# Optimization experiments

Measured on AMD Instinct MI355X. Metric: run time of the kernel, lower is better.

The kernel has to match this reference:

```python
import math
import jax, jax.numpy as jnp
import numpy as np

B, H, W, C = 2, 32, 32, 64
K = 15
G = 4
GC = C // G
K2 = K * K
RED = C // 4
MAX_SIGMA = 0.5


def setup_inputs() -> dict:
    key = jax.random.key(0)
    ks = jax.random.split(key, 32)
    f32 = jnp.float32

    def rn(k, shape, std):
        return (jax.random.normal(k, shape) * std).astype(f32)

    lin = 1.0 / math.sqrt(C)
    inp = {
        'x': jax.random.normal(ks[0], (B, H, W, C), f32),
        'raw_sigma': jnp.asarray(math.log(math.exp(0.3) - 1.0), f32),
        'base_offset_scale': jnp.asarray(0.1, f32),
        # input/output projections (stored [in,out])
        'w_ip': rn(ks[1], (C, C), lin), 'b_ip': jnp.zeros((C,), f32),
        'w_op': rn(ks[2], (C, C), lin), 'b_op': jnp.zeros((C,), f32),
        # dw_conv: depthwise 3x3 (HWIO, I=1) then pointwise 1x1 ([in,out])
        'w_dw': rn(ks[3], (3, 3, 1, C), 1.0 / 3.0), 'b_dw': jnp.zeros((C,), f32),
        'w_pw': rn(ks[4], (C, C), lin), 'b_pw': jnp.zeros((C,), f32),
        # offset / mask heads (original zero-inits; small random to exercise path)
        'w_off': rn(ks[5], (C, G * K2 * 2), 0.01), 'b_off': rn(ks[6], (G * K2 * 2,), 0.01),
        'w_msk': rn(ks[7], (C, G * K2), 0.01), 'b_msk': rn(ks[8], (G * K2,), 0.01),
        # kernel MLP: 2 -> 32 -> 32 -> G*GC
        'w_k1': rn(ks[9], (2, 32), 0.5), 'b_k1': jnp.zeros((32,), f32),
        'w_k2': rn(ks[10], (32, 32), 1.0 / math.sqrt(32)), 'b_k2': jnp.zeros((32,), f32),
        'w_k3': rn(ks[11], (32, G * GC), 1.0 / math.sqrt(32)), 'b_k3': jnp.zeros((G * GC,), f32),
        # SE block
        'w_fc1': rn(ks[12], (C, RED), lin), 'b_fc1': jnp.zeros((RED,), f32),
        'w_fc2': rn(ks[13], (RED, C), 1.0 / math.sqrt(RED)), 'b_fc2': jnp.zeros((C,), f32),
    }
    return inp


def _forward(x, raw_sigma, base_offset_scale, w_ip, b_ip, w_op, b_op, w_dw, b_dw,
             w_pw, b_pw, w_off, b_off, w_msk, b_msk, w_k1, b_k1, w_k2, b_k2,
             w_k3, b_k3, w_fc1, b_fc1, w_fc2, b_fc2):
    Bx, Hx, Wx, Cx = x.shape
    sigma = jnp.clip(jax.nn.softplus(raw_sigma), 1e-3, MAX_SIGMA)
    grid = jnp.linspace(-0.5, 0.5, K)  # [K]

    x_proj = x @ w_ip + b_ip  # [B,H,W,C]

    # depthwise 3x3 (SAME) + SiLU + pointwise 1x1
    y = jax.lax.conv_general_dilated(
        x, w_dw, (1, 1), 'SAME',
        dimension_numbers=('NHWC', 'HWIO', 'NHWC'), feature_group_count=Cx) + b_dw
    x_dw = jax.nn.silu(y) @ w_pw + b_pw  # [B,H,W,C]

    # Gaussian envelope over kernel grid, normalized
    env = jnp.exp(-(grid[:, None] ** 2 + grid[None, :] ** 2) / (2.0 * sigma ** 2))
    env = env / jnp.maximum(env.sum(), 1e-8)
    env_flat = env.reshape(1, 1, 1, 1, K2)

    gh, gw = jnp.meshgrid(grid, grid, indexing='ij')
    pos = jnp.stack([gh.ravel(), gw.ravel()], axis=-1) * 2.0  # [K2,2]
    hkw = jax.nn.silu(pos @ w_k1 + b_k1)
    hkw = jax.nn.silu(hkw @ w_k2 + b_k2)
    kw_raw = hkw @ w_k3 + b_k3  # [K2, G*GC]
    # faithful to torch view quirk: (K,K,G,gc) memory reinterpreted as (G,K2,gc)
    kw = kw_raw.reshape(G, K2, GC).reshape(1, 1, 1, G, K2, GC)

    offsets = (x_dw @ w_off + b_off).reshape(Bx, Hx, Wx, G, K2, 2) * base_offset_scale
    raw_mask = (x_dw @ w_msk + b_msk).reshape(Bx, Hx, Wx, G, K2) * env_flat
    attn = jnp.nan_to_num(jax.nn.softmax(raw_mask, axis=-1))

    # absolute sampling locations
    ref = jnp.linspace(-(K // 2), K // 2, K)
    rh, rw = jnp.meshgrid(ref, ref, indexing='ij')  # [K,K]
    pos_h = jnp.arange(Hx, dtype=x.dtype).reshape(1, Hx, 1, 1, 1)
    pos_w = jnp.arange(Wx, dtype=x.dtype).reshape(1, 1, Wx, 1, 1)
    abs_h = pos_h + rh.ravel().reshape(1, 1, 1, 1, K2) + offsets[..., 0]
    abs_w = pos_w + rw.ravel().reshape(1, 1, 1, 1, K2) + offsets[..., 1]
    ah = jnp.clip(abs_h, 0.0, Hx - 1)
    aw = jnp.clip(abs_w, 0.0, Wx - 1)
    h_f = jnp.clip(jnp.floor(ah).astype(jnp.int32), 0, Hx - 1)
    w_f = jnp.clip(jnp.floor(aw).astype(jnp.int32), 0, Wx - 1)
    h_c = jnp.minimum(h_f + 1, Hx - 1)
    w_c = jnp.minimum(w_f + 1, Wx - 1)
    hw = ah - h_f.astype(x.dtype)
    ww = aw - w_f.astype(x.dtype)
    valid = (~((abs_h < 0) | (abs_h > Hx - 1) | (abs_w < 0) | (abs_w > Wx - 1))).astype(x.dtype)

    xg = x_proj.reshape(Bx, Hx, Wx, G, GC)
    b_idx = jnp.arange(Bx).reshape(Bx, 1, 1, 1, 1)
    g_idx = jnp.arange(G).reshape(1, 1, 1, G, 1)
    v_ff = xg[b_idx, h_f, w_f, g_idx]  # [B,H,W,G,K2,GC]
    v_fc = xg[b_idx, h_f, w_c, g_idx]
    v_cf = xg[b_idx, h_c, w_f, g_idx]
    v_cc = xg[b_idx, h_c, w_c, g_idx]
    sampled = (v_ff * ((1 - hw) * (1 - ww) * valid)[..., None]
               + v_fc * ((1 - hw) * ww * valid)[..., None]
               + v_cf * (hw * (1 - ww) * valid)[..., None]
               + v_cc * (hw * ww * valid)[..., None])
    sampled = sampled * kw
    output = (sampled * attn[..., None]).sum(axis=4).reshape(Bx, Hx, Wx, Cx)

    # SE block (no mask, no bias)
    pooled = output.mean(axis=(1, 2), keepdims=True)
    se = jax.nn.silu(pooled @ w_fc1 + b_fc1) @ w_fc2 + b_fc2
    output = output * jax.nn.sigmoid(se)

    out = output @ w_op + b_op
    offset_reg = (offsets ** 2).mean()
    entropy = -(attn * jnp.log(attn + 1e-8)).sum(axis=-1).mean()
    return out, offset_reg, -entropy


def reference(x, raw_sigma, base_offset_scale, w_ip, b_ip, w_op, b_op, w_dw, b_dw,
              w_pw, b_pw, w_off, b_off, w_msk, b_msk, w_k1, b_k1, w_k2, b_k2,
              w_k3, b_k3, w_fc1, b_fc1, w_fc2, b_fc2):
    return _forward(x, raw_sigma, base_offset_scale, w_ip, b_ip, w_op, b_op,
                    w_dw, b_dw, w_pw, b_pw, w_off, b_off, w_msk, b_msk,
                    w_k1, b_k1, w_k2, b_k2, w_k3, b_k3, w_fc1, b_fc1, w_fc2, b_fc2)
```

## Files before the change

kernel.cpp:

```cpp
#include <hip/hip_runtime.h>
#include <math.h>

#define KK2 225
#define NPIX 2048
#define OFFC 1800
#define MSKC 900
#define NCOL 2700
#define NCOLP 2704
#define HSTR 2704

#define WROW 17
#define WCOL 20
#define WPOS (WROW*WCOL)
#define WSTR 68

#define WS_KW    0
#define WS_XPROJ 16384
#define WS_XB    (16384+131072)
#define WS_OUT   (16384+2*131072)
#define WS_POOL  (16384+3*131072)
#define WS_GATE  (WS_POOL+128)
#define WS_ENTP  (WS_GATE+128)
#define WS_OFFP  (WS_ENTP+2048)
#define WS_PART2 (WS_OFFP+512)
#define WS_WB    (WS_PART2+4096)
#define WS_HD    (WS_WB+86528)

typedef __attribute__((ext_vector_type(8))) short short8;
typedef __attribute__((ext_vector_type(4))) float f32x4;

__device__ __forceinline__ float silu(float a) { return a / (1.f + __expf(-a)); }
__device__ __forceinline__ unsigned short f2bf(float f) {
  unsigned u = __float_as_uint(f);
  u += 0x7FFFu + ((u >> 16) & 1u);
  return (unsigned short)(u >> 16);
}
__device__ __forceinline__ float bf2f(unsigned short h) {
  return __uint_as_float(((unsigned)h) << 16);
}

__global__ __launch_bounds__(256) void k_pre(
    const float* __restrict__ x,
    const float* __restrict__ w_ip, const float* __restrict__ b_ip,
    const float* __restrict__ w_dw, const float* __restrict__ b_dw,
    const float* __restrict__ w_pw, const float* __restrict__ b_pw,
    const float* __restrict__ w_k1, const float* __restrict__ b_k1,
    const float* __restrict__ w_k2, const float* __restrict__ b_k2,
    const float* __restrict__ w_k3, const float* __restrict__ b_k3,
    const float* __restrict__ w_off, const float* __restrict__ w_msk,
    float* __restrict__ ws)
{
  int t = threadIdx.x;
  if (blockIdx.x < 512) {
    int px = t >> 6, c = t & 63;
    int pix = blockIdx.x * 4 + px;
    int b = pix >> 10, h = (pix >> 5) & 31, w = pix & 31;
    __shared__ float xs[4][64], ys[4][64];
    xs[px][c] = x[pix*64 + c];
    float acc = b_dw[c];
    #pragma unroll
    for (int dh = -1; dh <= 1; dh++) {
      int hh = h + dh;
      if (hh < 0 || hh > 31) continue;
      #pragma unroll
      for (int dw2 = -1; dw2 <= 1; dw2++) {
        int wp = w + dw2;
        if (wp < 0 || wp > 31) continue;
        acc += x[(((b*32 + hh)*32 + wp) << 6) + c] * w_dw[((dh+1)*3 + (dw2+1))*64 + c];
      }
    }
    ys[px][c] = silu(acc);
    __syncthreads();
    float p1 = b_ip[c], p2 = b_pw[c];
    #pragma unroll 8
    for (int k = 0; k < 64; k++) {
      p1 += xs[px][k] * w_ip[k*64 + c];
      p2 += ys[px][k] * w_pw[k*64 + c];
    }
    ((unsigned short*)(ws + WS_XPROJ))[pix*64 + c] = f2bf(p1);
    ((unsigned short*)(ws + WS_XB))[pix*64 + c]    = f2bf(p2);
  } else if (blockIdx.x < 569) {
    __shared__ float h1s[4][32], h2s[4][32];
    int tl = t >> 6, lane = t & 63;
    int tap = (blockIdx.x - 512) * 4 + tl;
    int tapc = min(tap, KK2 - 1);
    int i = tapc / 15, j = tapc % 15;
    float gi = -0.5f + (float)i * (1.0f/14.0f);
    float gj = -0.5f + (float)j * (1.0f/14.0f);
    float p0 = gi * 2.f, p1 = gj * 2.f;
    if (lane < 32) {
      float a = p0 * w_k1[lane] + p1 * w_k1[32 + lane] + b_k1[lane];
      h1s[tl][lane] = silu(a);
    }
    __syncthreads();
    if (lane < 32) {
      float a = b_k2[lane];
      #pragma unroll
      for (int q = 0; q < 32; q++) a += h1s[tl][q] * w_k2[q*32 + lane];
      h2s[tl][lane] = silu(a);
    }
    __syncthreads();
    float a = b_k3[lane];
    #pragma unroll
    for (int q = 0; q < 32; q++) a += h2s[tl][q] * w_k3[q*64 + lane];
    if (tap < KK2) ws[WS_KW + tap*64 + lane] = a;
  } else {
    unsigned short* wb = (unsigned short*)(ws + WS_WB);
    int cb = blockIdx.x - 569;
    int col = cb*16 + (t & 15);
    int kk = (t >> 4) * 4;
    unsigned short v4[4];
    #pragma unroll
    for (int j = 0; j < 4; j++) {
      int k = kk + j;
      float v = 0.f;
      if (col < OFFC)      v = w_off[k*OFFC + col];
      else if (col < NCOL) v = w_msk[k*MSKC + col - OFFC];
      v4[j] = f2bf(v);
    }
    *(uint2*)&wb[(size_t)col*64 + kk] = *(uint2*)v4;
  }
}

__global__ __launch_bounds__(256) void k_gemm(
    const float* __restrict__ base_scale,
    const float* __restrict__ b_off, const float* __restrict__ b_msk,
    float* __restrict__ ws)
{
  int t = threadIdx.x;
  int wv = t >> 6, lane = t & 63;
  int row = lane & 15, rg = lane >> 4;
  int k0 = rg * 8;
  int colb = blockIdx.x * 64;
  int pxb  = blockIdx.y * 64 + wv * 16;
  const unsigned short* xb = (const unsigned short*)(ws + WS_XB);
  const unsigned short* wb = (const unsigned short*)(ws + WS_WB);
  unsigned short* hd = (unsigned short*)(ws + WS_HD);
  float scale = base_scale[0];

  short8 a_lo = *(const short8*)&xb[(size_t)(pxb + row)*64 + k0];
  short8 a_hi = *(const short8*)&xb[(size_t)(pxb + row)*64 + k0 + 32];
  #pragma unroll
  for (int ct = 0; ct < 4; ct++) {
    int c0 = colb + ct*16;
    if (c0 >= NCOLP) break;
    const short8 b_lo = *(const short8*)&wb[(size_t)(c0 + row)*64 + k0];
    const short8 b_hi = *(const short8*)&wb[(size_t)(c0 + row)*64 + k0 + 32];
    f32x4 acc = {0.f, 0.f, 0.f, 0.f};
    acc = __builtin_amdgcn_mfma_f32_16x16x32_bf16(a_lo, b_lo, acc, 0, 0, 0);
    acc = __builtin_amdgcn_mfma_f32_16x16x32_bf16(a_hi, b_hi, acc, 0, 0, 0);
    int col = c0 + row;
    float bias = 0.f, mult = 1.f;
    if (col < OFFC)      { bias = b_off[col]; mult = scale; }
    else if (col < NCOL) { bias = b_msk[col - OFFC]; }
    #pragma unroll
    for (int r = 0; r < 4; r++) {
      int px = pxb + rg*4 + r;
      hd[(size_t)px*HSTR + col] = f2bf((acc[r] + bias) * mult);
    }
  }
}

__global__ __launch_bounds__(1024, 8) void k_samp(
    const float* __restrict__ raw_sigma,
    float* __restrict__ ws)
{
  __shared__ unsigned short uni[WPOS*WSTR];
  __shared__ float env_s[KK2];
  __shared__ float red_s[16];
  __shared__ float ent_sh[16];
  __shared__ float env_sum;

  int t = threadIdx.x;
  int wv = t >> 6, lane = t & 63;
  int pix0 = blockIdx.x * 4;
  int b = pix0 >> 10;
  int h0 = (pix0 >> 5) & 31, w0 = pix0 & 31;
  const unsigned short* hd = (const unsigned short*)(ws + WS_HD);

  float sp = log1pf(__expf(raw_sigma[0]));
  float sigma = fminf(fmaxf(sp, 1e-3f), 0.5f);
  float envv = 0.f;
  if (t < KK2) {
    int i = t / 15, j = t % 15;
    float gi = -0.5f + (float)i * (1.0f/14.0f);
    float gj = -0.5f + (float)j * (1.0f/14.0f);
    envv = __expf(-(gi*gi + gj*gj) / (2.f*sigma*sigma));
  }
  {
    float v = envv;
    #pragma unroll
    for (int m = 32; m > 0; m >>= 1) v += __shfl_xor(v, m);
    if (lane == 0) red_s[wv] = v;
    __syncthreads();
    if (t == 0) {
      float s = 0.f;
      #pragma unroll
      for (int q = 0; q < 16; q++) s += red_s[q];
      env_sum = fmaxf(s, 1e-8f);
    }
    __syncthreads();
    if (t < KK2) env_s[t] = envv / env_sum;
  }

  {
    const unsigned short* xpb = (const unsigned short*)(ws + WS_XPROJ) + ((size_t)(b << 10) << 6);
    for (int idx = t; idx < WPOS*16; idx += 1024) {
      int pos = idx >> 4, c4 = idx & 15;
      int r = pos / WCOL, c = pos - r*WCOL;
      int sh = min(max(h0 - 8 + r, 0), 31);
      int sw = min(max(w0 - 8 + c, 0), 31);
      uint2 u = *(const uint2*)&xpb[((sh*32 + sw) << 6) + c4*4];
      *(uint2*)&uni[pos*WSTR + c4*4] = u;
    }
  }

  int spx = wv >> 2, g = wv & 3;
  const unsigned short* hrow = hd + (size_t)(pix0 + spx)*HSTR;
  float v[4];
  {
    float m = -INFINITY;
    #pragma unroll
    for (int kk = 0; kk < 4; kk++) {
      int p = lane + kk*64;
      if (p < KK2) { v[kk] = bf2f(hrow[OFFC + g*KK2 + p]) * env_s[p]; m = fmaxf(m, v[kk]); }
      else v[kk] = -INFINITY;
    }
    #pragma unroll
    for (int s = 32; s > 0; s >>= 1) m = fmaxf(m, __shfl_xor(m, s));
    float sum = 0.f;
    #pragma unroll
    for (int kk = 0; kk < 4; kk++) {
      int p = lane + kk*64;
      if (p < KK2) { v[kk] = __expf(v[kk] - m); sum += v[kk]; }
    }
    #pragma unroll
    for (int s = 32; s > 0; s >>= 1) sum += __shfl_xor(sum, s);
    float inv = 1.f / sum;
    float ent = 0.f;
    #pragma unroll
    for (int kk = 0; kk < 4; kk++) {
      int p = lane + kk*64;
      if (p < KK2) {
        float a = v[kk] * inv;
        v[kk] = a;
        ent += a * __logf(a + 1e-8f);
      }
    }
    #pragma unroll
    for (int s = 32; s > 0; s >>= 1) ent += __shfl_xor(ent, s);
    if (lane == 0) ent_sh[wv] = ent;
  }
  __syncthreads();
  if (t < 4) ws[WS_ENTP + pix0 + t] =
      ent_sh[t*4] + ent_sh[t*4+1] + ent_sh[t*4+2] + ent_sh[t*4+3];

  float offreg = 0.f;
  {
    int ts = lane >> 2, cl = lane & 3;
    int wpx = w0 + spx;
    int chbase = g*16 + cl*4;
    const float* kwg = ws + WS_KW + g*3600 + cl*4;
    float4 acc = make_float4(0.f, 0.f, 0.f, 0.f);
    #pragma unroll
    for (int kq = 0; kq < 4; kq++) {
      float av = v[kq];
      int nIt = (kq == 3) ? 3 : 4;
      #pragma unroll 1
      for (int i2 = 0; i2 < nIt; i2++) {
        int p = kq*64 + i2*16 + ts;
        if (p < KK2) {
          float at = __shfl(av, i2*16 + ts);
          unsigned op = *(const unsigned*)&hrow[g*450 + p*2];
          float o0 = bf2f((unsigned short)(op & 0xFFFFu));
          float o1 = bf2f((unsigned short)(op >> 16));
          if (cl == 0) offreg += o0*o0 + o1*o1;
          int pr = p / 15, pc = p - pr*15;
          float abs_h = (float)(h0 + pr - 7) + o0;
          float abs_w = (float)(wpx + pc - 7) + o1;
          float ah = fminf(fmaxf(abs_h, 0.f), 31.f);
          float aw = fminf(fmaxf(abs_w, 0.f), 31.f);
          int hf = (int)ah;
          int wf = (int)aw;
          float hw_ = ah - (float)hf, ww_ = aw - (float)wf;
          int rf = hf - h0 + 8;
          int rc = min(hf + 1, 31) - h0 + 8;
          int cf = wf - w0 + 8;
          int cc = min(wf + 1, 31) - w0 + 8;
          float s = (abs_h < 0.f || abs_h > 31.f || abs_w < 0.f || abs_w > 31.f) ? 0.f : at;
          float w00 = (1.f-hw_)*(1.f-ww_)*s, w01 = (1.f-hw_)*ww_*s;
          float w10 = hw_*(1.f-ww_)*s,       w11 = hw_*ww_*s;
          uint2 qff = *(const uint2*)&uni[(rf*WCOL + cf)*WSTR + chbase];
          uint2 qfc = *(const uint2*)&uni[(rf*WCOL + cc)*WSTR + chbase];
          uint2 qcf = *(const uint2*)&uni[(rc*WCOL + cf)*WSTR + chbase];
          uint2 qcc = *(const uint2*)&uni[(rc*WCOL + cc)*WSTR + chbase];
          float4 kwv = *(const float4*)&kwg[p*16];
          float ff0 = __uint_as_float(qff.x << 16), ff1 = __uint_as_float(qff.x & 0xFFFF0000u);
          float ff2 = __uint_as_float(qff.y << 16), ff3 = __uint_as_float(qff.y & 0xFFFF0000u);
          float fc0 = __uint_as_float(qfc.x << 16), fc1 = __uint_as_float(qfc.x & 0xFFFF0000u);
          float fc2 = __uint_as_float(qfc.y << 16), fc3 = __uint_as_float(qfc.y & 0xFFFF0000u);
          float cf0 = __uint_as_float(qcf.x << 16), cf1 = __uint_as_float(qcf.x & 0xFFFF0000u);
          float cf2 = __uint_as_float(qcf.y << 16), cf3 = __uint_as_float(qcf.y & 0xFFFF0000u);
          float cc0 = __uint_as_float(qcc.x << 16), cc1 = __uint_as_float(qcc.x & 0xFFFF0000u);
          float cc2 = __uint_as_float(qcc.y << 16), cc3 = __uint_as_float(qcc.y & 0xFFFF0000u);
          acc.x += (ff0*w00 + fc0*w01 + cf0*w10 + cc0*w11) * kwv.x;
          acc.y += (ff1*w00 + fc1*w01 + cf1*w10 + cc1*w11) * kwv.y;
          acc.z += (ff2*w00 + fc2*w01 + cf2*w10 + cc2*w11) * kwv.z;
          acc.w += (ff3*w00 + fc3*w01 + cf3*w10 + cc3*w11) * kwv.w;
        }
      }
    }
    #pragma unroll
    for (int m = 4; m < 64; m <<= 1) {
      acc.x += __shfl_xor(acc.x, m);
      acc.y += __shfl_xor(acc.y, m);
      acc.z += __shfl_xor(acc.z, m);
      acc.w += __shfl_xor(acc.w, m);
    }
    if (lane < 4) *(float4*)&ws[WS_OUT + (pix0 + spx)*64 + g*16 + cl*4] = acc;
  }
  {
    #pragma unroll
    for (int m = 32; m > 0; m >>= 1) offreg += __shfl_xor(offreg, m);
    if (lane == 0) red_s[wv] = offreg;
    __syncthreads();
    if (t == 0) {
      float s = 0.f;
      #pragma unroll
      for (int q = 0; q < 16; q++) s += red_s[q];
      ws[WS_OFFP + blockIdx.x] = s;
    }
  }
}

__global__ __launch_bounds__(256) void k_red(float* __restrict__ ws, float* __restrict__ d_out)
{
  __shared__ float red[256];
  int t = threadIdx.x, blk = blockIdx.x;
  if (blk < 64) {
    int b = blk >> 5, chunk = blk & 31;
    int c = t & 63, str = t >> 6;
    const float* base = ws + WS_OUT + (size_t)((b*1024 + chunk*32) << 6) + c;
    float s = 0.f;
    #pragma unroll
    for (int i = 0; i < 8; i++) s += base[((str + i*4) << 6)];
    red[t] = s;
    __syncthreads();
    if (t < 64) ws[WS_PART2 + blk*64 + t] =
      red[t] + red[t+64] + red[t+128] + red[t+192];
  } else if (blk == 64) {
    float s = 0.f;
    #pragma unroll
    for (int i = 0; i < 8; i++) s += ws[WS_ENTP + t + i*256];
    #pragma unroll
    for (int m = 32; m > 0; m >>= 1) s += __shfl_xor(s, m);
    if ((t & 63) == 0) red[t >> 6] = s;
    __syncthreads();
    if (t == 0) d_out[NPIX*64 + 1] = (red[0] + red[1] + red[2] + red[3]) * (1.f/8192.f);
  } else {
    float s = 0.f;
    #pragma unroll
    for (int i = 0; i < 2; i++) s += ws[WS_OFFP + t + i*256];
    #pragma unroll
    for (int m = 32; m > 0; m >>= 1) s += __shfl_xor(s, m);
    if ((t & 63) == 0) red[t >> 6] = s;
    __syncthreads();
    if (t == 0) d_out[NPIX*64] = (red[0] + red[1] + red[2] + red[3]) * (1.f/3686400.f);
  }
}

__global__ __launch_bounds__(128) void k_se(
    const float* __restrict__ w_fc1, const float* __restrict__ b_fc1,
    const float* __restrict__ w_fc2, const float* __restrict__ b_fc2,
    float* __restrict__ ws)
{
  __shared__ float pool_s[2][64];
  __shared__ float hsh[2][16];
  int t = threadIdx.x;
  int b = t >> 6, c = t & 63;
  {
    float s = 0.f;
    #pragma unroll
    for (int ch = 0; ch < 32; ch++) s += ws[WS_PART2 + (b*32 + ch)*64 + c];
    pool_s[b][c] = s * (1.f/1024.f);
  }
  __syncthreads();
  if (t < 32) {
    int bb = t >> 4, r = t & 15;
    float a = b_fc1[r];
    #pragma unroll 16
    for (int cc = 0; cc < 64; cc++) a += pool_s[bb][cc] * w_fc1[cc*16 + r];
    hsh[bb][r] = silu(a);
  }
  __syncthreads();
  float a = b_fc2[c];
  #pragma unroll
  for (int r = 0; r < 16; r++) a += hsh[b][r] * w_fc2[r*64 + c];
  ws[WS_GATE + b*64 + c] = 1.f / (1.f + __expf(-a));
}

__global__ __launch_bounds__(256) void k_final(
    const float* __restrict__ w_op, const float* __restrict__ b_op,
    const float* __restrict__ ws, float* __restrict__ d_out)
{
  int t = threadIdx.x;
  int px = t >> 6, c = t & 63;
  int pix = blockIdx.x * 4 + px;
  int b = pix >> 10;
  __shared__ float sc[4][64];
  sc[px][c] = ws[WS_OUT + pix*64 + c] * ws[WS_GATE + b*64 + c];
  __syncthreads();
  float a = b_op[c];
  #pragma unroll 8
  for (int k = 0; k < 64; k++) a += sc[px][k] * w_op[k*64 + c];
  d_out[pix*64 + c] = a;
}

extern "C" void kernel_launch(void* const* d_in, const int* in_sizes, int n_in,
                              void* d_out, int out_size, void* d_ws, size_t ws_size,
                              hipStream_t stream)
{
  const float* x     = (const float*)d_in[0];
  const float* rsig  = (const float*)d_in[1];
  const float* bos   = (const float*)d_in[2];
  const float* w_ip  = (const float*)d_in[3];
  const float* b_ip  = (const float*)d_in[4];
  const float* w_op  = (const float*)d_in[5];
  const float* b_op  = (const float*)d_in[6];
  const float* w_dw  = (const float*)d_in[7];
  const float* b_dw  = (const float*)d_in[8];
  const float* w_pw  = (const float*)d_in[9];
  const float* b_pw  = (const float*)d_in[10];
  const float* w_off = (const float*)d_in[11];
  const float* b_off = (const float*)d_in[12];
  const float* w_msk = (const float*)d_in[13];
  const float* b_msk = (const float*)d_in[14];
  const float* w_k1  = (const float*)d_in[15];
  const float* b_k1  = (const float*)d_in[16];
  const float* w_k2  = (const float*)d_in[17];
  const float* b_k2  = (const float*)d_in[18];
  const float* w_k3  = (const float*)d_in[19];
  const float* b_k3  = (const float*)d_in[20];
  const float* w_fc1 = (const float*)d_in[21];
  const float* b_fc1 = (const float*)d_in[22];
  const float* w_fc2 = (const float*)d_in[23];
  const float* b_fc2 = (const float*)d_in[24];
  float* ws  = (float*)d_ws;
  float* out = (float*)d_out;

  hipLaunchKernelGGL(k_pre, dim3(738), dim3(256), 0, stream,
                     x, w_ip, b_ip, w_dw, b_dw, w_pw, b_pw,
                     w_k1, b_k1, w_k2, b_k2, w_k3, b_k3, w_off, w_msk, ws);
  hipLaunchKernelGGL(k_gemm, dim3(43, 32), dim3(256), 0, stream,
                     bos, b_off, b_msk, ws);
  hipLaunchKernelGGL(k_samp, dim3(512), dim3(1024), 0, stream,
                     rsig, ws);
  hipLaunchKernelGGL(k_red, dim3(66), dim3(256), 0, stream, ws, out);
  hipLaunchKernelGGL(k_se, dim3(1), dim3(128), 0, stream,
                     w_fc1, b_fc1, w_fc2, b_fc2, ws);
  hipLaunchKernelGGL(k_final, dim3(512), dim3(256), 0, stream,
                     w_op, b_op, ws, out);
}
```

Baseline: 59.23 us.

## Fold reduction kernel into sampler and SE, stage offsets in LDS, bf16 kernel weights

Drops the separate k_red launch. k_samp now writes per-block channel partial sums, and k_se (grown to 1024 threads) reduces those partials plus the entropy and offset-regularizer scalars. Inside k_samp, each block's offsets are staged into shared memory once and the offset-regularizer is computed there, instead of reading global memory per tap. The sampling loop is flattened to 15 iterations with partial unroll, and the dynamic-kernel weights are stored as bf16. This removes one launch and some global traffic, at the cost of more LDS per block (reducing occupancy) and lower precision in the kernel weights.

New measurement: 56.64 us. 4.4% less time.

```diff
diff --git a/kernel.cpp b/kernel.cpp
--- a/kernel.cpp
+++ b/kernel.cpp
@@ -14,17 +14,16 @@
 #define WPOS (WROW*WCOL)
 #define WSTR 68
 
-#define WS_KW    0
+#define WS_KWB   0
 #define WS_XPROJ 16384
-#define WS_XB    (16384+131072)
-#define WS_OUT   (16384+2*131072)
-#define WS_POOL  (16384+3*131072)
-#define WS_GATE  (WS_POOL+128)
-#define WS_ENTP  (WS_GATE+128)
-#define WS_OFFP  (WS_ENTP+2048)
-#define WS_PART2 (WS_OFFP+512)
-#define WS_WB    (WS_PART2+4096)
-#define WS_HD    (WS_WB+86528)
+#define WS_XB    81920
+#define WS_OUT   147456
+#define WS_GATE  278528
+#define WS_ENTP  278656
+#define WS_OFFP  280704
+#define WS_PART2 281216
+#define WS_WB    313984
+#define WS_HD    400512
 
 typedef __attribute__((ext_vector_type(8))) short short8;
 typedef __attribute__((ext_vector_type(4))) float f32x4;
@@ -103,7 +102,7 @@
     float a = b_k3[lane];
     #pragma unroll
     for (int q = 0; q < 32; q++) a += h2s[tl][q] * w_k3[q*64 + lane];
-    if (tap < KK2) ws[WS_KW + tap*64 + lane] = a;
+    if (tap < KK2) ((unsigned short*)(ws + WS_KWB))[tap*64 + lane] = f2bf(a);
   } else {
     unsigned short* wb = (unsigned short*)(ws + WS_WB);
     int cb = blockIdx.x - 569;
@@ -166,6 +165,8 @@
     float* __restrict__ ws)
 {
   __shared__ unsigned short uni[WPOS*WSTR];
+  __shared__ unsigned short off_s[4*OFFC];
+  __shared__ float po_s[4][64];
   __shared__ float env_s[KK2];
   __shared__ float red_s[16];
   __shared__ float ent_sh[16];
@@ -203,6 +204,23 @@
     if (t < KK2) env_s[t] = envv / env_sum;
   }
 
+  float offreg = 0.f;
+  {
+    for (int idx = t; idx < 1800; idx += 1024) {
+      int px = idx / 450, q = idx - px*450;
+      uint2 u = *(const uint2*)&hd[(size_t)(pix0 + px)*HSTR + q*4];
+      *(uint2*)&off_s[px*OFFC + q*4] = u;
+      float o0 = bf2f((unsigned short)(u.x & 0xFFFFu));
+      float o1 = bf2f((unsigned short)(u.x >> 16));
+      float o2 = bf2f((unsigned short)(u.y & 0xFFFFu));
+      float o3 = bf2f((unsigned short)(u.y >> 16));
+      offreg += o0*o0 + o1*o1 + o2*o2 + o3*o3;
+    }
+    #pragma unroll
+    for (int m = 32; m > 0; m >>= 1) offreg += __shfl_xor(offreg, m);
+    if (lane == 0) red_s[wv] = offreg;
+  }
+
   {
     const unsigned short* xpb = (const unsigned short*)(ws + WS_XPROJ) + ((size_t)(b << 10) << 6);
     for (int idx = t; idx < WPOS*16; idx += 1024) {
@@ -214,6 +232,13 @@
       *(uint2*)&uni[pos*WSTR + c4*4] = u;
     }
   }
+  __syncthreads();
+  if (t == 0) {
+    float s = 0.f;
+    #pragma unroll
+    for (int q = 0; q < 16; q++) s += red_s[q];
+    ws[WS_OFFP + blockIdx.x] = s;
+  }
 
   int spx = wv >> 2, g = wv & 3;
   const unsigned short* hrow = hd + (size_t)(pix0 + spx)*HSTR;
@@ -251,63 +276,58 @@
     for (int s = 32; s > 0; s >>= 1) ent += __shfl_xor(ent, s);
     if (lane == 0) ent_sh[wv] = ent;
   }
-  __syncthreads();
-  if (t < 4) ws[WS_ENTP + pix0 + t] =
-      ent_sh[t*4] + ent_sh[t*4+1] + ent_sh[t*4+2] + ent_sh[t*4+3];
-
-  float offreg = 0.f;
+
   {
     int ts = lane >> 2, cl = lane & 3;
     int wpx = w0 + spx;
     int chbase = g*16 + cl*4;
-    const float* kwg = ws + WS_KW + g*3600 + cl*4;
+    const unsigned short* kwb = (const unsigned short*)(ws + WS_KWB);
+    int kwbase = g*3600 + cl*4;
     float4 acc = make_float4(0.f, 0.f, 0.f, 0.f);
-    #pragma unroll
-    for (int kq = 0; kq < 4; kq++) {
-      float av = v[kq];
-      int nIt = (kq == 3) ? 3 : 4;
-      #pragma unroll 1
-      for (int i2 = 0; i2 < nIt; i2++) {
-        int p = kq*64 + i2*16 + ts;
-        if (p < KK2) {
-          float at = __shfl(av, i2*16 + ts);
-          unsigned op = *(const unsigned*)&hrow[g*450 + p*2];
-          float o0 = bf2f((unsigned short)(op & 0xFFFFu));
-          float o1 = bf2f((unsigned short)(op >> 16));
-          if (cl == 0) offreg += o0*o0 + o1*o1;
-          int pr = p / 15, pc = p - pr*15;
-          float abs_h = (float)(h0 + pr - 7) + o0;
-          float abs_w = (float)(wpx + pc - 7) + o1;
-          float ah = fminf(fmaxf(abs_h, 0.f), 31.f);
-          float aw = fminf(fmaxf(abs_w, 0.f), 31.f);
-          int hf = (int)ah;
-          int wf = (int)aw;
-          float hw_ = ah - (float)hf, ww_ = aw - (float)wf;
-          int rf = hf - h0 + 8;
-          int rc = min(hf + 1, 31) - h0 + 8;
-          int cf = wf - w0 + 8;
-          int cc = min(wf + 1, 31) - w0 + 8;
-          float s = (abs_h < 0.f || abs_h > 31.f || abs_w < 0.f || abs_w > 31.f) ? 0.f : at;
-          float w00 = (1.f-hw_)*(1.f-ww_)*s, w01 = (1.f-hw_)*ww_*s;
-          float w10 = hw_*(1.f-ww_)*s,       w11 = hw_*ww_*s;
-          uint2 qff = *(const uint2*)&uni[(rf*WCOL + cf)*WSTR + chbase];
-          uint2 qfc = *(const uint2*)&uni[(rf*WCOL + cc)*WSTR + chbase];
-          uint2 qcf = *(const uint2*)&uni[(rc*WCOL + cf)*WSTR + chbase];
-          uint2 qcc = *(const uint2*)&uni[(rc*WCOL + cc)*WSTR + chbase];
-          float4 kwv = *(const float4*)&kwg[p*16];
-          float ff0 = __uint_as_float(qff.x << 16), ff1 = __uint_as_float(qff.x & 0xFFFF0000u);
-          float ff2 = __uint_as_float(qff.y << 16), ff3 = __uint_as_float(qff.y & 0xFFFF0000u);
-          float fc0 = __uint_as_float(qfc.x << 16), fc1 = __uint_as_float(qfc.x & 0xFFFF0000u);
-          float fc2 = __uint_as_float(qfc.y << 16), fc3 = __uint_as_float(qfc.y & 0xFFFF0000u);
-          float cf0 = __uint_as_float(qcf.x << 16), cf1 = __uint_as_float(qcf.x & 0xFFFF0000u);
-          float cf2 = __uint_as_float(qcf.y << 16), cf3 = __uint_as_float(qcf.y & 0xFFFF0000u);
-          float cc0 = __uint_as_float(qcc.x << 16), cc1 = __uint_as_float(qcc.x & 0xFFFF0000u);
-          float cc2 = __uint_as_float(qcc.y << 16), cc3 = __uint_as_float(qcc.y & 0xFFFF0000u);
-          acc.x += (ff0*w00 + fc0*w01 + cf0*w10 + cc0*w11) * kwv.x;
-          acc.y += (ff1*w00 + fc1*w01 + cf1*w10 + cc1*w11) * kwv.y;
-          acc.z += (ff2*w00 + fc2*w01 + cf2*w10 + cc2*w11) * kwv.z;
-          acc.w += (ff3*w00 + fc3*w01 + cf3*w10 + cc3*w11) * kwv.w;
-        }
+    #pragma unroll 5
+    for (int k = 0; k < 15; k++) {
+      int p = ts + k*16;
+      if (p < KK2) {
+        float at = __shfl(v[k >> 2], ts + ((k & 3) << 4));
+        unsigned op = *(const unsigned*)&off_s[spx*OFFC + g*450 + p*2];
+        float o0 = bf2f((unsigned short)(op & 0xFFFFu));
+        float o1 = bf2f((unsigned short)(op >> 16));
+        int pr = p / 15, pc = p - pr*15;
+        float abs_h = (float)(h0 + pr - 7) + o0;
+        float abs_w = (float)(wpx + pc - 7) + o1;
+        float ah = fminf(fmaxf(abs_h, 0.f), 31.f);
+        float aw = fminf(fmaxf(abs_w, 0.f), 31.f);
+        int hf = (int)ah;
+        int wf = (int)aw;
+        float hw_ = ah - (float)hf, ww_ = aw - (float)wf;
+        int rf = hf - h0 + 8;
+        int rc = min(hf + 1, 31) - h0 + 8;
+        int cf = wf - w0 + 8;
+        int cc = min(wf + 1, 31) - w0 + 8;
+        float s = (abs_h < 0.f || abs_h > 31.f || abs_w < 0.f || abs_w > 31.f) ? 0.f : at;
+        float w00 = (1.f-hw_)*(1.f-ww_)*s, w01 = (1.f-hw_)*ww_*s;
+        float w10 = hw_*(1.f-ww_)*s,       w11 = hw_*ww_*s;
+        uint2 qff = *(const uint2*)&uni[(rf*WCOL + cf)*WSTR + chbase];
+        uint2 qfc = *(const uint2*)&uni[(rf*WCOL + cc)*WSTR + chbase];
+        uint2 qcf = *(const uint2*)&uni[(rc*WCOL + cf)*WSTR + chbase];
+        uint2 qcc = *(const uint2*)&uni[(rc*WCOL + cc)*WSTR + chbase];
+        uint2 kq = *(const uint2*)&kwb[kwbase + p*16];
+        float kw0 = bf2f((unsigned short)(kq.x & 0xFFFFu));
+        float kw1 = bf2f((unsigned short)(kq.x >> 16));
+        float kw2 = bf2f((unsigned short)(kq.y & 0xFFFFu));
+        float kw3 = bf2f((unsigned short)(kq.y >> 16));
+        float ff0 = __uint_as_float(qff.x << 16), ff1 = __uint_as_float(qff.x & 0xFFFF0000u);
+        float ff2 = __uint_as_float(qff.y << 16), ff3 = __uint_as_float(qff.y & 0xFFFF0000u);
+        float fc0 = __uint_as_float(qfc.x << 16), fc1 = __uint_as_float(qfc.x & 0xFFFF0000u);
+        float fc2 = __uint_as_float(qfc.y << 16), fc3 = __uint_as_float(qfc.y & 0xFFFF0000u);
+        float cf0 = __uint_as_float(qcf.x << 16), cf1 = __uint_as_float(qcf.x & 0xFFFF0000u);
+        float cf2 = __uint_as_float(qcf.y << 16), cf3 = __uint_as_float(qcf.y & 0xFFFF0000u);
+        float cc0 = __uint_as_float(qcc.x << 16), cc1 = __uint_as_float(qcc.x & 0xFFFF0000u);
+        float cc2 = __uint_as_float(qcc.y << 16), cc3 = __uint_as_float(qcc.y & 0xFFFF0000u);
+        acc.x += (ff0*w00 + fc0*w01 + cf0*w10 + cc0*w11) * kw0;
+        acc.y += (ff1*w00 + fc1*w01 + cf1*w10 + cc1*w11) * kw1;
+        acc.z += (ff2*w00 + fc2*w01 + cf2*w10 + cc2*w11) * kw2;
+        acc.w += (ff3*w00 + fc3*w01 + cf3*w10 + cc3*w11) * kw3;
       }
     }
     #pragma unroll
@@ -317,72 +337,59 @@
       acc.z += __shfl_xor(acc.z, m);
       acc.w += __shfl_xor(acc.w, m);
     }
-    if (lane < 4) *(float4*)&ws[WS_OUT + (pix0 + spx)*64 + g*16 + cl*4] = acc;
-  }
-  {
-    #pragma unroll
-    for (int m = 32; m > 0; m >>= 1) offreg += __shfl_xor(offreg, m);
-    if (lane == 0) red_s[wv] = offreg;
-    __syncthreads();
-    if (t == 0) {
-      float s = 0.f;
-      #pragma unroll
-      for (int q = 0; q < 16; q++) s += red_s[q];
-      ws[WS_OFFP + blockIdx.x] = s;
-    }
-  }
-}
-
-__global__ __launch_bounds__(256) void k_red(float* __restrict__ ws, float* __restrict__ d_out)
-{
-  __shared__ float red[256];
-  int t = threadIdx.x, blk = blockIdx.x;
-  if (blk < 64) {
-    int b = blk >> 5, chunk = blk & 31;
-    int c = t & 63, str = t >> 6;
-    const float* base = ws + WS_OUT + (size_t)((b*1024 + chunk*32) << 6) + c;
-    float s = 0.f;
-    #pragma unroll
-    for (int i = 0; i < 8; i++) s += base[((str + i*4) << 6)];
-    red[t] = s;
-    __syncthreads();
-    if (t < 64) ws[WS_PART2 + blk*64 + t] =
-      red[t] + red[t+64] + red[t+128] + red[t+192];
-  } else if (blk == 64) {
-    float s = 0.f;
-    #pragma unroll
-    for (int i = 0; i < 8; i++) s += ws[WS_ENTP + t + i*256];
-    #pragma unroll
-    for (int m = 32; m > 0; m >>= 1) s += __shfl_xor(s, m);
-    if ((t & 63) == 0) red[t >> 6] = s;
-    __syncthreads();
-    if (t == 0) d_out[NPIX*64 + 1] = (red[0] + red[1] + red[2] + red[3]) * (1.f/8192.f);
-  } else {
-    float s = 0.f;
-    #pragma unroll
-    for (int i = 0; i < 2; i++) s += ws[WS_OFFP + t + i*256];
-    #pragma unroll
-    for (int m = 32; m > 0; m >>= 1) s += __shfl_xor(s, m);
-    if ((t & 63) == 0) red[t >> 6] = s;
-    __syncthreads();
-    if (t == 0) d_out[NPIX*64] = (red[0] + red[1] + red[2] + red[3]) * (1.f/3686400.f);
-  }
-}
-
-__global__ __launch_bounds__(128) void k_se(
+    if (lane < 4) {
+      *(float4*)&ws[WS_OUT + (pix0 + spx)*64 + g*16 + cl*4] = acc;
+      *(float4*)&po_s[spx][g*16 + cl*4] = acc;
+    }
+  }
+  __syncthreads();
+  if (t < 64) ws[WS_PART2 + blockIdx.x*64 + t] =
+      po_s[0][t] + po_s[1][t] + po_s[2][t] + po_s[3][t];
+  if (t < 4) ws[WS_ENTP + pix0 + t] =
+      ent_sh[t*4] + ent_sh[t*4+1] + ent_sh[t*4+2] + ent_sh[t*4+3];
+}
+
+__global__ __launch_bounds__(1024) void k_se(
     const float* __restrict__ w_fc1, const float* __restrict__ b_fc1,
     const float* __restrict__ w_fc2, const float* __restrict__ b_fc2,
-    float* __restrict__ ws)
-{
+    float* __restrict__ ws, float* __restrict__ d_out)
+{
+  __shared__ float redm[16][64];
   __shared__ float pool_s[2][64];
   __shared__ float hsh[2][16];
+  __shared__ float rscal[32];
   int t = threadIdx.x;
-  int b = t >> 6, c = t & 63;
-  {
+  int wv = t >> 6, lane = t & 63;
+  int c = lane;
+  {
+    int b = wv & 1, seg = wv >> 1;
     float s = 0.f;
     #pragma unroll
-    for (int ch = 0; ch < 32; ch++) s += ws[WS_PART2 + (b*32 + ch)*64 + c];
-    pool_s[b][c] = s * (1.f/1024.f);
+    for (int i = 0; i < 32; i++)
+      s += ws[WS_PART2 + (((b*256 + seg*32 + i) << 6) + c)];
+    redm[wv][c] = s;
+  }
+  {
+    float e = ws[WS_ENTP + t] + ws[WS_ENTP + t + 1024];
+    float o = (t < 512) ? ws[WS_OFFP + t] : 0.f;
+    #pragma unroll
+    for (int m = 32; m > 0; m >>= 1) { e += __shfl_xor(e, m); o += __shfl_xor(o, m); }
+    if (lane == 0) { rscal[wv] = e; rscal[16 + wv] = o; }
+  }
+  __syncthreads();
+  if (t < 128) {
+    int bb = t >> 6, cc = t & 63;
+    float s2 = 0.f;
+    #pragma unroll
+    for (int seg = 0; seg < 8; seg++) s2 += redm[seg*2 + bb][cc];
+    pool_s[bb][cc] = s2 * (1.f/1024.f);
+  }
+  if (t == 0) {
+    float se_ = 0.f, so = 0.f;
+    #pragma unroll
+    for (int q = 0; q < 16; q++) { se_ += rscal[q]; so += rscal[16 + q]; }
+    d_out[NPIX*64 + 1] = se_ * (1.f/8192.f);
+    d_out[NPIX*64]     = so  * (1.f/3686400.f);
   }
   __syncthreads();
   if (t < 32) {
@@ -393,10 +400,13 @@
     hsh[bb][r] = silu(a);
   }
   __syncthreads();
-  float a = b_fc2[c];
-  #pragma unroll
-  for (int r = 0; r < 16; r++) a += hsh[b][r] * w_fc2[r*64 + c];
-  ws[WS_GATE + b*64 + c] = 1.f / (1.f + __expf(-a));
+  if (t < 128) {
+    int bb = t >> 6, cc = t & 63;
+    float a = b_fc2[cc];
+    #pragma unroll
+    for (int r = 0; r < 16; r++) a += hsh[bb][r] * w_fc2[r*64 + cc];
+    ws[WS_GATE + bb*64 + cc] = 1.f / (1.f + __expf(-a));
+  }
 }
 
 __global__ __launch_bounds__(256) void k_final(
@@ -455,9 +465,8 @@
                      bos, b_off, b_msk, ws);
   hipLaunchKernelGGL(k_samp, dim3(512), dim3(1024), 0, stream,
                      rsig, ws);
-  hipLaunchKernelGGL(k_red, dim3(66), dim3(256), 0, stream, ws, out);
-  hipLaunchKernelGGL(k_se, dim3(1), dim3(128), 0, stream,
-                     w_fc1, b_fc1, w_fc2, b_fc2, ws);
+  hipLaunchKernelGGL(k_se, dim3(1), dim3(1024), 0, stream,
+                     w_fc1, b_fc1, w_fc2, b_fc2, ws, out);
   hipLaunchKernelGGL(k_final, dim3(512), dim3(256), 0, stream,
                      w_op, b_op, ws, out);
 }
```
